# Kernel tuning notes

Hardware: AMD Instinct MI355X
Metric: run time of the kernel (lower is better)

The kernel has to match this reference:

```python
import jax, jax.numpy as jnp
import numpy as np

N, S, EMBED, LATENT, HVGS, E = 8192, 128, 256, 128, 2000, 131072


def setup_inputs() -> dict:
    key = jax.random.key(0)
    ks = jax.random.split(key, 12)
    sd = lambda fan_in: 1.0 / np.sqrt(fan_in)
    inp = {
        "emb": jax.random.normal(ks[0], (N, S, EMBED), dtype=jnp.float32),
        "edge_index": jax.random.randint(ks[1], (2, E), 0, N, dtype=jnp.int64),
        "Wq": jax.random.uniform(ks[2], (EMBED, LATENT), jnp.float32, -sd(EMBED), sd(EMBED)),
        "bq": jnp.zeros((LATENT,), jnp.float32),
        "Wk": jax.random.uniform(ks[3], (EMBED, LATENT), jnp.float32, -sd(EMBED), sd(EMBED)),
        "bk": jnp.zeros((LATENT,), jnp.float32),
        "Wv": jax.random.uniform(ks[4], (EMBED, LATENT), jnp.float32, -sd(EMBED), sd(EMBED)),
        "bv": jnp.zeros((LATENT,), jnp.float32),
        "Wo": jax.random.uniform(ks[5], (LATENT, LATENT), jnp.float32, -sd(LATENT), sd(LATENT)),
        "bo": jnp.zeros((LATENT,), jnp.float32),
        "Wg": jax.random.uniform(ks[6], (LATENT, HVGS), jnp.float32, -sd(LATENT), sd(LATENT)),
        "bg": jnp.zeros((HVGS,), jnp.float32),
    }
    return inp


def _gcn(x, W, b, edge_index):
    # PyG GCNConv with add_self_loops=True, symmetric normalization
    h = x @ W  # [N, HVGS]
    n = x.shape[0]
    loop = jnp.arange(n, dtype=edge_index.dtype)
    src = jnp.concatenate([edge_index[0], loop])
    dst = jnp.concatenate([edge_index[1], loop])
    deg = jax.ops.segment_sum(jnp.ones_like(src, dtype=h.dtype), dst, num_segments=n)
    dinv = jnp.where(deg > 0, jax.lax.rsqrt(deg), 0.0)
    norm = dinv[src] * dinv[dst]  # [E+N]
    out = jax.ops.segment_sum(h[src] * norm[:, None], dst, num_segments=n)
    return out + b


def reference(emb, edge_index, Wq, bq, Wk, bk, Wv, bv, Wo, bo, Wg, bg):
    Q = emb @ Wq + bq  # [N, S, L]
    K = emb @ Wk + bk
    V = emb @ Wv + bv
    scale = 1.0 / np.sqrt(emb.shape[-1])
    att_weights = jnp.tanh(jnp.einsum("nsl,ntl->nst", Q, K) * scale)  # [N, S, S]
    att_out = jnp.einsum("nst,ntl->nsl", att_weights, V)
    z = (att_out @ Wo + bo).mean(axis=1)  # [N, L]
    output = _gcn(z, Wg, bg, edge_index)  # [N, HVGS]
    return (att_weights, z, output)
```

## Files before the change

kernel.cpp:

```cpp
#include <hip/hip_runtime.h>
#include <cstdint>
#include <cstddef>

#define NN   8192
#define SS   128
#define EMBD 256
#define LL   128
#define HV   2000
#define EE   131072

typedef float  f32x4  __attribute__((ext_vector_type(4)));
typedef __bf16 bf16x8 __attribute__((ext_vector_type(8)));
typedef unsigned int   u32x4 __attribute__((ext_vector_type(4)));
typedef unsigned short u16x4 __attribute__((ext_vector_type(4)));

__device__ __forceinline__ unsigned short f2bf(float f) {
  unsigned u; __builtin_memcpy(&u, &f, 4);
  unsigned r = u + 0x7fffu + ((u >> 16) & 1u);
  return (unsigned short)(r >> 16);
}

__global__ void prep_w(const float* __restrict__ Wq, const float* __restrict__ Wk,
                       unsigned short* __restrict__ wT) {
  int idx = blockIdx.x * 256 + threadIdx.x;
  int c = idx >> 8, e = idx & 255;
  float v = (c < 128) ? Wq[(size_t)e * LL + c] : Wk[(size_t)e * LL + (c - 128)];
  wT[idx] = f2bf(v);
}

#define PJ_LDS 32768
__global__ __launch_bounds__(512, 2)
void proj(const float* __restrict__ emb, const unsigned short* __restrict__ wT,
          const float* __restrict__ bq, const float* __restrict__ bk,
          float* __restrict__ qkOut)
{
  extern __shared__ char lds[];
  unsigned short* sE = (unsigned short*)lds;

  const int blk  = blockIdx.x;
  const int n    = blk >> 1;
  const int s0   = (blk & 1) * 64;
  const int tid  = threadIdx.x;
  const int wid  = tid >> 6;
  const int lane = tid & 63;
  const int lx   = lane & 15;
  const int g    = lane >> 4;
  const int sw   = (lx & 7) << 3;

  {
    const f32x4* src = (const f32x4*)(emb + ((size_t)n * SS + s0) * EMBD);
    #pragma unroll
    for (int it = 0; it < 8; it++) {
      int i = it * 512 + tid;
      f32x4 v = src[i];
      int s = i >> 6, e0 = (i & 63) << 2;
      u16x4 h;
      h[0] = f2bf(v[0]); h[1] = f2bf(v[1]); h[2] = f2bf(v[2]); h[3] = f2bf(v[3]);
      *(u16x4*)(sE + s * 256 + (e0 ^ ((s & 7) << 3))) = h;
    }
  }
  __syncthreads();

  const int col0 = (wid << 5) + lx;
  u32x4 Bfr[2][8];
  #pragma unroll
  for (int n2 = 0; n2 < 2; n2++)
    #pragma unroll
    for (int ks = 0; ks < 8; ks++)
      Bfr[n2][ks] = *(const u32x4*)(wT + (size_t)(col0 + n2 * 16) * 256 + ks * 32 + g * 8);

  float b0 = (col0 < 128) ? bq[col0] : bk[col0 - 128];
  float b1 = (col0 + 16 < 128) ? bq[col0 + 16] : bk[col0 + 16 - 128];

  f32x4 acc[4][2];
  #pragma unroll
  for (int m = 0; m < 4; m++) { acc[m][0] = f32x4{0,0,0,0}; acc[m][1] = f32x4{0,0,0,0}; }

  #pragma unroll
  for (int m = 0; m < 4; m++) {
    u32x4 A[8];
    #pragma unroll
    for (int ks = 0; ks < 8; ks++)
      A[ks] = *(const u32x4*)(sE + (m * 16 + lx) * 256 + ((ks * 32 + g * 8) ^ sw));
    #pragma unroll
    for (int ks = 0; ks < 8; ks++) {
      acc[m][0] = __builtin_amdgcn_mfma_f32_16x16x32_bf16(
                    __builtin_bit_cast(bf16x8, A[ks]), __builtin_bit_cast(bf16x8, Bfr[0][ks]),
                    acc[m][0], 0, 0, 0);
      acc[m][1] = __builtin_amdgcn_mfma_f32_16x16x32_bf16(
                    __builtin_bit_cast(bf16x8, A[ks]), __builtin_bit_cast(bf16x8, Bfr[1][ks]),
                    acc[m][1], 0, 0, 0);
    }
  }
  __syncthreads();

  #pragma unroll
  for (int m = 0; m < 4; m++) {
    #pragma unroll
    for (int n2 = 0; n2 < 2; n2++) {
      const int col = col0 + n2 * 16;
      const float bb = n2 ? b1 : b0;
      #pragma unroll
      for (int r = 0; r < 4; r++) {
        const int srow = m * 16 + g * 4 + r;
        sE[srow * 256 + (col ^ ((srow & 7) << 3))] = f2bf(acc[m][n2][r] + bb);
      }
    }
  }
  __syncthreads();

  {
    f32x4* dst = (f32x4*)(qkOut + (size_t)n * (SS * SS) + (size_t)s0 * 128);
    const f32x4* s4 = (const f32x4*)sE;
    #pragma unroll
    for (int it = 0; it < 4; it++) dst[it * 512 + tid] = s4[it * 512 + tid];
  }
}

#define AT_LDS (65536 + 4096)
__global__ __launch_bounds__(512, 2)
void attn(float* __restrict__ attIO, float* __restrict__ cOut)
{
  extern __shared__ char lds[];
  unsigned short* sQK = (unsigned short*)lds;
  float* scr = (float*)(lds + 65536);

  const int n    = blockIdx.x;
  const int tid  = threadIdx.x;
  const int wid  = tid >> 6;
  const int lane = tid & 63;
  const int lx   = lane & 15;
  const int g    = lane >> 4;
  const int sw   = (lx & 7) << 3;

  float* slot = attIO + (size_t)n * (SS * SS);

  {
    const u32x4* src = (const u32x4*)slot;
    u32x4* dst = (u32x4*)sQK;
    #pragma unroll
    for (int it = 0; it < 8; it++) dst[it * 512 + tid] = src[it * 512 + tid];
  }
  __syncthreads();

  bf16x8 qf[4];
  #pragma unroll
  for (int ks = 0; ks < 4; ks++)
    qf[ks] = __builtin_bit_cast(bf16x8,
      *(const u32x4*)(sQK + (wid * 16 + lx) * 256 + ((ks * 32 + g * 8) ^ sw)));

  f32x4 accS[8];
  #pragma unroll
  for (int nt = 0; nt < 8; nt++) accS[nt] = f32x4{0,0,0,0};
  #pragma unroll
  for (int nt = 0; nt < 8; nt++) {
    const int tr = nt * 16 + lx;
    #pragma unroll
    for (int ks = 0; ks < 4; ks++) {
      u32x4 t = *(const u32x4*)(sQK + tr * 256 + 128 + ((ks * 32 + g * 8) ^ sw));
      accS[nt] = __builtin_amdgcn_mfma_f32_16x16x32_bf16(
                   qf[ks], __builtin_bit_cast(bf16x8, t), accS[nt], 0, 0, 0);
    }
  }

  {
    const int srow0 = wid * 16 + g * 4;
    float colp[8];
    #pragma unroll
    for (int nt = 0; nt < 8; nt++) {
      float p = 0.f;
      #pragma unroll
      for (int r = 0; r < 4; r++) {
        float x  = accS[nt][r] * 0.0625f;
        float ax = fabsf(x);
        float ex = __expf(ax * 2.0f);
        float th = __builtin_copysignf(__fdividef(ex - 1.0f, ex + 1.0f), x);
        p += th;
        slot[(size_t)(srow0 + r) * SS + nt * 16 + lx] = th;
      }
      p += __shfl_xor(p, 16, 64);
      p += __shfl_xor(p, 32, 64);
      colp[nt] = p;
    }
    if (lane < 16) {
      #pragma unroll
      for (int nt = 0; nt < 8; nt++) scr[wid * 128 + nt * 16 + lane] = colp[nt];
    }
  }
  __syncthreads();

  if (tid < 128) {
    float s = 0.f;
    #pragma unroll
    for (int w = 0; w < 8; w++) s += scr[w * 128 + tid];
    cOut[(size_t)n * 128 + tid] = s * (1.0f / 128.0f);
  }
}

__global__ __launch_bounds__(256)
void zker(const float* __restrict__ emb, const float* __restrict__ cIn,
          const float* __restrict__ Wv, const float* __restrict__ bv,
          const float* __restrict__ Wo, const float* __restrict__ bo,
          float* __restrict__ zOut)
{
  __shared__ float cS[128], ceS[256], mS[128], scr2[256], csS[2];
  const int n = blockIdx.x, tid = threadIdx.x;

  if (tid < 128) {
    float c = cIn[(size_t)n * 128 + tid];
    cS[tid] = c;
    float r = c;
    #pragma unroll
    for (int off = 32; off >= 1; off >>= 1) r += __shfl_down(r, off, 64);
    if ((tid & 63) == 0) csS[tid >> 6] = r;
  }
  __syncthreads();

  {
    const float* e = emb + (size_t)n * (SS * EMBD) + tid;
    float acc = 0.f;
    #pragma unroll 8
    for (int t = 0; t < 128; t++) acc += cS[t] * e[(size_t)t * EMBD];
    ceS[tid] = acc;
  }
  __syncthreads();

  {
    const int l = tid & 127, h = tid >> 7;
    float a = 0.f;
    #pragma unroll 8
    for (int i = 0; i < 128; i++)
      a += ceS[h * 128 + i] * Wv[(size_t)(h * 128 + i) * LL + l];
    scr2[tid] = a;
  }
  __syncthreads();
  if (tid < 128) {
    float csum = csS[0] + csS[1];
    mS[tid] = scr2[tid] + scr2[128 + tid] + csum * bv[tid];
  }
  __syncthreads();

  {
    const int j = tid & 127, h = tid >> 7;
    float a = 0.f;
    #pragma unroll 8
    for (int i = 0; i < 64; i++)
      a += mS[h * 64 + i] * Wo[(size_t)(h * 64 + i) * LL + j];
    scr2[tid] = a;
  }
  __syncthreads();
  if (tid < 128)
    zOut[(size_t)n * LL + tid] = scr2[tid] + scr2[128 + tid] + bo[tid];
}

__global__ void gcn_deg(const int* __restrict__ eidx, float* __restrict__ deg) {
  int e = blockIdx.x * 256 + threadIdx.x;
  if (e < EE) atomicAdd(&deg[eidx[EE + e]], 1.0f);
}

__global__ void gcn_dinv(const float* __restrict__ deg, float* __restrict__ dinv) {
  int i = blockIdx.x * 256 + threadIdx.x;
  if (i < NN) dinv[i] = rsqrtf(deg[i] + 1.0f);
}

__global__ void gcn_self(const float* __restrict__ dinv, const float* __restrict__ z,
                         float* __restrict__ agg) {
  size_t gidx = (size_t)blockIdx.x * 256 + threadIdx.x;
  int i = (int)(gidx >> 7);
  float di = dinv[i];
  agg[gidx] = di * di * z[gidx];
}

__global__ void gcn_scatter(const int* __restrict__ eidx, const float* __restrict__ dinv,
                            const float* __restrict__ z, float* __restrict__ agg) {
  int w    = (blockIdx.x * blockDim.x + threadIdx.x) >> 6;
  int lane = threadIdx.x & 63;
  int nw   = (gridDim.x * blockDim.x) >> 6;
  for (int e = w; e < EE; e += nw) {
    int s = eidx[e], d = eidx[EE + e];
    float nrm = dinv[s] * dinv[d];
    atomicAdd(&agg[(size_t)d * 128 + lane],      nrm * z[(size_t)s * 128 + lane]);
    atomicAdd(&agg[(size_t)d * 128 + 64 + lane], nrm * z[(size_t)s * 128 + 64 + lane]);
  }
}

__global__ __launch_bounds__(256)
void out_gemm(const float* __restrict__ agg, const float* __restrict__ Wg,
              const float* __restrict__ bg, float* __restrict__ outp) {
  __shared__ float sA[8 * 128];
  const int nb = blockIdx.x * 8;
  const int tid = threadIdx.x;
  {
    const float4* src = (const float4*)(agg + (size_t)nb * 128);
    ((float4*)sA)[tid] = src[tid];
  }
  __syncthreads();
  const int g0 = tid * 8;
  if (g0 < HV) {
    float acc[8][8];
    #pragma unroll
    for (int i = 0; i < 8; i++)
      #pragma unroll
      for (int j = 0; j < 8; j++) acc[i][j] = 0.0f;
    #pragma unroll 2
    for (int l = 0; l < 128; l++) {
      float4 wa = *(const float4*)(Wg + (size_t)l * HV + g0);
      float4 wb = *(const float4*)(Wg + (size_t)l * HV + g0 + 4);
      float w[8] = {wa.x, wa.y, wa.z, wa.w, wb.x, wb.y, wb.z, wb.w};
      #pragma unroll
      for (int i = 0; i < 8; i++) {
        float a = sA[i * 128 + l];
        #pragma unroll
        for (int j = 0; j < 8; j++) acc[i][j] += a * w[j];
      }
    }
    float b[8];
    #pragma unroll
    for (int j = 0; j < 8; j++) b[j] = bg[g0 + j];
    #pragma unroll
    for (int i = 0; i < 8; i++) {
      float4 oa = make_float4(acc[i][0] + b[0], acc[i][1] + b[1], acc[i][2] + b[2], acc[i][3] + b[3]);
      float4 ob = make_float4(acc[i][4] + b[4], acc[i][5] + b[5], acc[i][6] + b[6], acc[i][7] + b[7]);
      *(float4*)(outp + (size_t)(nb + i) * HV + g0)     = oa;
      *(float4*)(outp + (size_t)(nb + i) * HV + g0 + 4) = ob;
    }
  }
}

extern "C" void kernel_launch(void* const* d_in, const int* in_sizes, int n_in,
                              void* d_out, int out_size, void* d_ws, size_t ws_size,
                              hipStream_t stream) {
  const float* emb  = (const float*)d_in[0];
  const int*   eidx = (const int*)d_in[1];
  const float* Wq = (const float*)d_in[2];
  const float* bq = (const float*)d_in[3];
  const float* Wk = (const float*)d_in[4];
  const float* bk = (const float*)d_in[5];
  const float* Wv = (const float*)d_in[6];
  const float* bv = (const float*)d_in[7];
  const float* Wo = (const float*)d_in[8];
  const float* bo = (const float*)d_in[9];
  const float* Wg = (const float*)d_in[10];
  const float* bg = (const float*)d_in[11];

  float* out  = (float*)d_out;
  float* attO = out;
  float* zO   = out + (size_t)NN * SS * SS;
  float* oO   = zO + (size_t)NN * LL;

  float* wsf  = (float*)d_ws;
  float* deg  = wsf;
  float* dinv = wsf + NN;
  float* agg  = wsf + 2 * NN;
  unsigned short* wT = (unsigned short*)(wsf + 2 * NN + (size_t)NN * 128);
  float* cWS  = wsf + 2 * NN + (size_t)NN * 128 + 32768;

  (void)in_sizes; (void)n_in; (void)out_size; (void)ws_size;

  hipFuncSetAttribute((const void*)proj,
                      hipFuncAttributeMaxDynamicSharedMemorySize, PJ_LDS);
  hipFuncSetAttribute((const void*)attn,
                      hipFuncAttributeMaxDynamicSharedMemorySize, AT_LDS);

  hipMemsetAsync(deg, 0, NN * sizeof(float), stream);
  gcn_deg <<<EE / 256, 256, 0, stream>>>(eidx, deg);
  gcn_dinv<<<NN / 256, 256, 0, stream>>>(deg, dinv);
  prep_w  <<<(2 * LL * EMBD) / 256, 256, 0, stream>>>(Wq, Wk, wT);

  proj<<<NN * 2, 512, PJ_LDS, stream>>>(emb, wT, bq, bk, attO);
  attn<<<NN, 512, AT_LDS, stream>>>(attO, cWS);
  zker<<<NN, 256, 0, stream>>>(emb, cWS, Wv, bv, Wo, bo, zO);

  gcn_self   <<<NN * 128 / 256, 256, 0, stream>>>(dinv, zO, agg);
  gcn_scatter<<<2048, 256, 0, stream>>>(eidx, dinv, zO, agg);
  out_gemm   <<<NN / 8, 256, 0, stream>>>(agg, Wg, bg, oO);
}
```

Baseline: 971.0 us.

## Fuse QK projection into attention kernel and vectorize zker emb reduction

Merges the proj and attn kernels into one qkatt kernel: each block loads one sample's embeddings, projects Q and K in two halves into LDS, then computes tanh attention directly. This drops the round trip of Q/K through the global attention output buffer. Separately, zker's c·emb reduction now uses f32x4 loads split across four row groups, followed by an LDS reduction. Costs: the fused kernel needs about 68KB of LDS per block, which limits occupancy, and the launch bound hint of 4 blocks per CU may raise register pressure.

```diff
diff --git a/kernel.cpp b/kernel.cpp
--- a/kernel.cpp
+++ b/kernel.cpp
@@ -28,101 +28,14 @@
   wT[idx] = f2bf(v);
 }
 
-#define PJ_LDS 32768
-__global__ __launch_bounds__(512, 2)
-void proj(const float* __restrict__ emb, const unsigned short* __restrict__ wT,
-          const float* __restrict__ bq, const float* __restrict__ bk,
-          float* __restrict__ qkOut)
+#define QA_LDS (65536 + 4096)
+__global__ __launch_bounds__(512, 4)
+void qkatt(const float* __restrict__ emb, const unsigned short* __restrict__ wT,
+           const float* __restrict__ bq, const float* __restrict__ bk,
+           float* __restrict__ attOut, float* __restrict__ cOut)
 {
   extern __shared__ char lds[];
   unsigned short* sE = (unsigned short*)lds;
-
-  const int blk  = blockIdx.x;
-  const int n    = blk >> 1;
-  const int s0   = (blk & 1) * 64;
-  const int tid  = threadIdx.x;
-  const int wid  = tid >> 6;
-  const int lane = tid & 63;
-  const int lx   = lane & 15;
-  const int g    = lane >> 4;
-  const int sw   = (lx & 7) << 3;
-
-  {
-    const f32x4* src = (const f32x4*)(emb + ((size_t)n * SS + s0) * EMBD);
-    #pragma unroll
-    for (int it = 0; it < 8; it++) {
-      int i = it * 512 + tid;
-      f32x4 v = src[i];
-      int s = i >> 6, e0 = (i & 63) << 2;
-      u16x4 h;
-      h[0] = f2bf(v[0]); h[1] = f2bf(v[1]); h[2] = f2bf(v[2]); h[3] = f2bf(v[3]);
-      *(u16x4*)(sE + s * 256 + (e0 ^ ((s & 7) << 3))) = h;
-    }
-  }
-  __syncthreads();
-
-  const int col0 = (wid << 5) + lx;
-  u32x4 Bfr[2][8];
-  #pragma unroll
-  for (int n2 = 0; n2 < 2; n2++)
-    #pragma unroll
-    for (int ks = 0; ks < 8; ks++)
-      Bfr[n2][ks] = *(const u32x4*)(wT + (size_t)(col0 + n2 * 16) * 256 + ks * 32 + g * 8);
-
-  float b0 = (col0 < 128) ? bq[col0] : bk[col0 - 128];
-  float b1 = (col0 + 16 < 128) ? bq[col0 + 16] : bk[col0 + 16 - 128];
-
-  f32x4 acc[4][2];
-  #pragma unroll
-  for (int m = 0; m < 4; m++) { acc[m][0] = f32x4{0,0,0,0}; acc[m][1] = f32x4{0,0,0,0}; }
-
-  #pragma unroll
-  for (int m = 0; m < 4; m++) {
-    u32x4 A[8];
-    #pragma unroll
-    for (int ks = 0; ks < 8; ks++)
-      A[ks] = *(const u32x4*)(sE + (m * 16 + lx) * 256 + ((ks * 32 + g * 8) ^ sw));
-    #pragma unroll
-    for (int ks = 0; ks < 8; ks++) {
-      acc[m][0] = __builtin_amdgcn_mfma_f32_16x16x32_bf16(
-                    __builtin_bit_cast(bf16x8, A[ks]), __builtin_bit_cast(bf16x8, Bfr[0][ks]),
-                    acc[m][0], 0, 0, 0);
-      acc[m][1] = __builtin_amdgcn_mfma_f32_16x16x32_bf16(
-                    __builtin_bit_cast(bf16x8, A[ks]), __builtin_bit_cast(bf16x8, Bfr[1][ks]),
-                    acc[m][1], 0, 0, 0);
-    }
-  }
-  __syncthreads();
-
-  #pragma unroll
-  for (int m = 0; m < 4; m++) {
-    #pragma unroll
-    for (int n2 = 0; n2 < 2; n2++) {
-      const int col = col0 + n2 * 16;
-      const float bb = n2 ? b1 : b0;
-      #pragma unroll
-      for (int r = 0; r < 4; r++) {
-        const int srow = m * 16 + g * 4 + r;
-        sE[srow * 256 + (col ^ ((srow & 7) << 3))] = f2bf(acc[m][n2][r] + bb);
-      }
-    }
-  }
-  __syncthreads();
-
-  {
-    f32x4* dst = (f32x4*)(qkOut + (size_t)n * (SS * SS) + (size_t)s0 * 128);
-    const f32x4* s4 = (const f32x4*)sE;
-    #pragma unroll
-    for (int it = 0; it < 4; it++) dst[it * 512 + tid] = s4[it * 512 + tid];
-  }
-}
-
-#define AT_LDS (65536 + 4096)
-__global__ __launch_bounds__(512, 2)
-void attn(float* __restrict__ attIO, float* __restrict__ cOut)
-{
-  extern __shared__ char lds[];
-  unsigned short* sQK = (unsigned short*)lds;
   float* scr = (float*)(lds + 65536);
 
   const int n    = blockIdx.x;
@@ -133,13 +46,67 @@
   const int g    = lane >> 4;
   const int sw   = (lx & 7) << 3;
 
-  float* slot = attIO + (size_t)n * (SS * SS);
-
-  {
-    const u32x4* src = (const u32x4*)slot;
-    u32x4* dst = (u32x4*)sQK;
-    #pragma unroll
-    for (int it = 0; it < 8; it++) dst[it * 512 + tid] = src[it * 512 + tid];
+  const float* embN = emb + (size_t)n * (SS * EMBD);
+
+  {
+    const f32x4* src = (const f32x4*)embN;
+    #pragma unroll
+    for (int it = 0; it < 16; it++) {
+      int i = it * 512 + tid;
+      f32x4 v = src[i];
+      int s = i >> 6, e0 = (i & 63) << 2;
+      u16x4 h;
+      h[0] = f2bf(v[0]); h[1] = f2bf(v[1]); h[2] = f2bf(v[2]); h[3] = f2bf(v[3]);
+      *(u16x4*)(sE + s * 256 + (e0 ^ ((s & 7) << 3))) = h;
+    }
+  }
+  __syncthreads();
+
+  const int col0 = (wid << 5) + lx;
+  float bias[2];
+  bias[0] = (col0      < 128) ? bq[col0]      : bk[col0 - 128];
+  bias[1] = (col0 + 16 < 128) ? bq[col0 + 16] : bk[col0 + 16 - 128];
+
+  #pragma unroll 1
+  for (int half = 0; half < 2; half++) {
+    f32x4 acc[2][4];
+    #pragma unroll
+    for (int n2 = 0; n2 < 2; n2++)
+      #pragma unroll
+      for (int m = 0; m < 4; m++) acc[n2][m] = f32x4{0.f, 0.f, 0.f, 0.f};
+
+    #pragma unroll
+    for (int n2 = 0; n2 < 2; n2++) {
+      u32x4 B[8];
+      const unsigned short* wp = wT + (size_t)(col0 + n2 * 16) * 256 + g * 8;
+      #pragma unroll
+      for (int ks = 0; ks < 8; ks++) B[ks] = *(const u32x4*)(wp + ks * 32);
+      #pragma unroll
+      for (int m = 0; m < 4; m++) {
+        const unsigned short* ap = sE + (half * 64 + m * 16 + lx) * 256;
+        #pragma unroll
+        for (int ks = 0; ks < 8; ks++) {
+          u32x4 A = *(const u32x4*)(ap + ((ks * 32 + g * 8) ^ sw));
+          acc[n2][m] = __builtin_amdgcn_mfma_f32_16x16x32_bf16(
+                         __builtin_bit_cast(bf16x8, A), __builtin_bit_cast(bf16x8, B[ks]),
+                         acc[n2][m], 0, 0, 0);
+        }
+      }
+    }
+    __syncthreads();
+
+    #pragma unroll
+    for (int n2 = 0; n2 < 2; n2++) {
+      const int col = col0 + n2 * 16;
+      const float bb = bias[n2];
+      #pragma unroll
+      for (int m = 0; m < 4; m++)
+        #pragma unroll
+        for (int r = 0; r < 4; r++) {
+          const int srow = half * 64 + m * 16 + g * 4 + r;
+          sE[srow * 256 + (col ^ ((srow & 7) << 3))] = f2bf(acc[n2][m][r] + bb);
+        }
+    }
   }
   __syncthreads();
 
@@ -147,23 +114,24 @@
   #pragma unroll
   for (int ks = 0; ks < 4; ks++)
     qf[ks] = __builtin_bit_cast(bf16x8,
-      *(const u32x4*)(sQK + (wid * 16 + lx) * 256 + ((ks * 32 + g * 8) ^ sw)));
+      *(const u32x4*)(sE + (wid * 16 + lx) * 256 + ((ks * 32 + g * 8) ^ sw)));
 
   f32x4 accS[8];
   #pragma unroll
-  for (int nt = 0; nt < 8; nt++) accS[nt] = f32x4{0,0,0,0};
+  for (int nt = 0; nt < 8; nt++) accS[nt] = f32x4{0.f, 0.f, 0.f, 0.f};
   #pragma unroll
   for (int nt = 0; nt < 8; nt++) {
     const int tr = nt * 16 + lx;
     #pragma unroll
     for (int ks = 0; ks < 4; ks++) {
-      u32x4 t = *(const u32x4*)(sQK + tr * 256 + 128 + ((ks * 32 + g * 8) ^ sw));
+      u32x4 t = *(const u32x4*)(sE + tr * 256 + 128 + ((ks * 32 + g * 8) ^ sw));
       accS[nt] = __builtin_amdgcn_mfma_f32_16x16x32_bf16(
                    qf[ks], __builtin_bit_cast(bf16x8, t), accS[nt], 0, 0, 0);
     }
   }
 
   {
+    float* slot = attOut + (size_t)n * (SS * SS);
     const int srow0 = wid * 16 + g * 4;
     float colp[8];
     #pragma unroll
@@ -203,7 +171,7 @@
           const float* __restrict__ Wo, const float* __restrict__ bo,
           float* __restrict__ zOut)
 {
-  __shared__ float cS[128], ceS[256], mS[128], scr2[256], csS[2];
+  __shared__ float cS[128], ceS[256], mS[128], scr2[256], csS[2], scrE[1024];
   const int n = blockIdx.x, tid = threadIdx.x;
 
   if (tid < 128) {
@@ -217,12 +185,17 @@
   __syncthreads();
 
   {
-    const float* e = emb + (size_t)n * (SS * EMBD) + tid;
-    float acc = 0.f;
+    const int h = tid >> 6, lane = tid & 63;
+    const f32x4* e4 = (const f32x4*)(emb + (size_t)n * (SS * EMBD));
+    f32x4 acc = f32x4{0.f, 0.f, 0.f, 0.f};
     #pragma unroll 8
-    for (int t = 0; t < 128; t++) acc += cS[t] * e[(size_t)t * EMBD];
-    ceS[tid] = acc;
-  }
+    for (int t = h; t < 128; t += 4)
+      acc += cS[t] * e4[(size_t)t * 64 + lane];
+    *(f32x4*)(scrE + h * 256 + lane * 4) = acc;
+  }
+  __syncthreads();
+  if (tid < 256)
+    ceS[tid] = scrE[tid] + scrE[256 + tid] + scrE[512 + tid] + scrE[768 + tid];
   __syncthreads();
 
   {
@@ -357,19 +330,16 @@
 
   (void)in_sizes; (void)n_in; (void)out_size; (void)ws_size;
 
-  hipFuncSetAttribute((const void*)proj,
-                      hipFuncAttributeMaxDynamicSharedMemorySize, PJ_LDS);
-  hipFuncSetAttribute((const void*)attn,
-                      hipFuncAttributeMaxDynamicSharedMemorySize, AT_LDS);
+  hipFuncSetAttribute((const void*)qkatt,
+                      hipFuncAttributeMaxDynamicSharedMemorySize, QA_LDS);
 
   hipMemsetAsync(deg, 0, NN * sizeof(float), stream);
   gcn_deg <<<EE / 256, 256, 0, stream>>>(eidx, deg);
   gcn_dinv<<<NN / 256, 256, 0, stream>>>(deg, dinv);
   prep_w  <<<(2 * LL * EMBD) / 256, 256, 0, stream>>>(Wq, Wk, wT);
 
-  proj<<<NN * 2, 512, PJ_LDS, stream>>>(emb, wT, bq, bk, attO);
-  attn<<<NN, 512, AT_LDS, stream>>>(attO, cWS);
-  zker<<<NN, 256, 0, stream>>>(emb, cWS, Wv, bv, Wo, bo, zO);
+  qkatt<<<NN, 512, QA_LDS, stream>>>(emb, wT, bq, bk, attO, cWS);
+  zker <<<NN, 256, 0, stream>>>(emb, cWS, Wv, bv, Wo, bo, zO);
 
   gcn_self   <<<NN * 128 / 256, 256, 0, stream>>>(dinv, zO, agg);
   gcn_scatter<<<2048, 256, 0, stream>>>(eidx, dinv, zO, agg);
```

Result: faster. 850.4 us (-12.4%).
